# Performance work log

Hardware: AMD Instinct MI355X
Metric: run time of the kernel (lower is better)

The kernel has to match this reference:

```python
import jax, jax.numpy as jnp
import numpy as np

ITERATIONS = 10      # skil_loss default
BORDER_SIZE = 25     # skil_loss default -> 51-tap gaussian
SIGMA = 10.0         # skil_loss default
LOSS_WEIGHT = 1.0
EPS = 1e-6


def _max_pool3(x):
    # 3x3 max pool, stride 1, SAME padding over last two dims of (N, H, W)
    return jax.lax.reduce_window(x, -jnp.inf, jax.lax.max,
                                 (1, 3, 3), (1, 1, 1), 'SAME')


def _soft_erode(x):
    return -_max_pool3(-x)


def _soft_dilate(x):
    return _max_pool3(x)


def _soft_open(x):
    return _soft_dilate(_soft_erode(x))


def soft_skeletonize(img, iterations):
    # clDice-style iterative soft skeletonization
    skel = jax.nn.relu(img - _soft_open(img))

    def body(carry, _):
        img, skel = carry
        img = _soft_erode(img)
        delta = jax.nn.relu(img - _soft_open(img))
        skel = skel + jax.nn.relu(delta - skel * delta)
        return (img, skel), None

    (img, skel), _ = jax.lax.scan(body, (img, skel), None, length=iterations)
    return skel


def apply_smooth_gaussian_diffusion(x, border_size, sigma):
    # Separable gaussian conv, kernel size 2*border_size+1, peak value 1
    # (soft dilation of the skeleton into a border band), clipped to [0, 1].
    r = jnp.arange(-border_size, border_size + 1, dtype=x.dtype)
    g = jnp.exp(-(r * r) / (2.0 * sigma * sigma))  # peak = 1 at center
    x4 = x[:, None, :, :]  # (N, 1, H, W)
    kh = g.reshape(1, 1, -1, 1)
    kw = g.reshape(1, 1, 1, -1)
    dn = ('NCHW', 'OIHW', 'NCHW')
    y = jax.lax.conv_general_dilated(x4, kh, (1, 1), 'SAME', dimension_numbers=dn)
    y = jax.lax.conv_general_dilated(y, kw, (1, 1), 'SAME', dimension_numbers=dn)
    return jnp.clip(y[:, 0], 0.0, 1.0)


def soft_dice(gt, pr, epsilon=EPS):
    num = 2.0 * jnp.sum(gt * pr, axis=(-2, -1))
    den = jnp.sum(gt * gt, axis=(-2, -1)) + jnp.sum(pr * pr, axis=(-2, -1))
    return (num + epsilon) / (den + epsilon)


def skil_loss(pred_fg, target):
    gt_skel = soft_skeletonize(target, ITERATIONS)
    pr_skel = soft_skeletonize(pred_fg, ITERATIONS)
    gt_border = apply_smooth_gaussian_diffusion(gt_skel, BORDER_SIZE, SIGMA)
    pr_border = apply_smooth_gaussian_diffusion(pr_skel, BORDER_SIZE, SIGMA)
    return 1.0 - soft_dice(gt_border, pr_border)  # (N,)


def setup_inputs() -> dict:
    key = jax.random.key(0)
    k1, k2 = jax.random.split(key)
    pred = jax.random.normal(k1, (8, 2, 1024, 1024), dtype=jnp.float32)
    target = jax.random.uniform(k2, (8, 1024, 1024), dtype=jnp.float32)
    return {"pred": pred, "target": target}


def reference(pred, target):
    # SkilLoss.forward: softmax over classes, foreground channel to skil_loss,
    # weighted_loss 'mean' reduction over batch.
    probs = jax.nn.softmax(pred, axis=1)
    fg = probs[:, 1]  # (N, H, W)
    loss = skil_loss(fg, target)
    return LOSS_WEIGHT * jnp.mean(loss)
```

## Files before the change

kernel.cpp:

```cpp
#include <hip/hip_runtime.h>

#define H 1024
#define W 1024
#define HW (H*W)
#define NB 8
#define NIMG 16
#define BORDER 25
#define KLEN 51

__device__ __constant__ float GW[KLEN] = {
  0.04393693f, 0.05613476f, 0.07100535f, 0.08892162f, 0.11025053f,
  0.13533528f, 0.16447446f, 0.19789869f, 0.23574608f, 0.27803730f,
  0.32465247f, 0.37531110f, 0.42955736f, 0.48675226f, 0.54607442f,
  0.60653066f, 0.66697681f, 0.72614904f, 0.78270454f, 0.83527021f,
  0.88249690f, 0.92311635f, 0.95599748f, 0.98019867f, 0.99501248f,
  1.00000000f,
  0.99501248f, 0.98019867f, 0.95599748f, 0.92311635f, 0.88249690f,
  0.83527021f, 0.78270454f, 0.72614904f, 0.66697681f, 0.60653066f,
  0.54607442f, 0.48675226f, 0.42955736f, 0.37531110f, 0.32465247f,
  0.27803730f, 0.23574608f, 0.19789869f, 0.16447446f, 0.13533528f,
  0.11025053f, 0.08892162f, 0.07100535f, 0.05613476f, 0.04393693f
};

__device__ inline float m3n(float a,float b,float c){
  float d; asm("v_min3_f32 %0, %1, %2, %3" : "=v"(d) : "v"(a), "v"(b), "v"(c));
  return d;
}
__device__ inline float m3x(float a,float b,float c){
  float d; asm("v_max3_f32 %0, %1, %2, %3" : "=v"(d) : "v"(a), "v"(b), "v"(c));
  return d;
}

__device__ inline float dpp_shr1(float x){
  return __int_as_float(__builtin_amdgcn_mov_dpp(__float_as_int(x), 0x138, 0xf, 0xf, true));
}
__device__ inline float dpp_shl1(float x){
  return __int_as_float(__builtin_amdgcn_mov_dpp(__float_as_int(x), 0x130, 0xf, 0xf, true));
}

__device__ inline float4 hmin4(float4 C){
  float Lw = dpp_shr1(C.w);
  float Rx = dpp_shl1(C.x);
  float4 h;
  h.x=m3n(Lw ,C.x,C.y); h.y=m3n(C.x,C.y,C.z);
  h.z=m3n(C.y,C.z,C.w); h.w=m3n(C.z,C.w,Rx );
  return h;
}
__device__ inline float4 hmax4(float4 C){
  float Lw = dpp_shr1(C.w);
  float Rx = dpp_shl1(C.x);
  float4 h;
  h.x=m3x(Lw ,C.x,C.y); h.y=m3x(C.x,C.y,C.z);
  h.z=m3x(C.y,C.z,C.w); h.w=m3x(C.z,C.w,Rx );
  return h;
}
__device__ inline float4 vmin3(float4 a,float4 b,float4 c){
  float4 o; o.x=m3n(a.x,b.x,c.x); o.y=m3n(a.y,b.y,c.y);
            o.z=m3n(a.z,b.z,c.z); o.w=m3n(a.w,b.w,c.w); return o;
}
__device__ inline float4 vmax3(float4 a,float4 b,float4 c){
  float4 o; o.x=m3x(a.x,b.x,c.x); o.y=m3x(a.y,b.y,c.y);
            o.z=m3x(a.z,b.z,c.z); o.w=m3x(a.w,b.w,c.w); return o;
}
__device__ inline float4 msk4(float4 e, bool v){
  constexpr float NINF = -__builtin_huge_valf();
  float4 o; o.x=v?e.x:NINF; o.y=v?e.y:NINF; o.z=v?e.z:NINF; o.w=v?e.w:NINF;
  return o;
}

__global__ __launch_bounds__(512, 4)
void skel11_kernel(const float* __restrict__ pred, const float* __restrict__ targ,
                   float* __restrict__ S, double* __restrict__ sums,
                   unsigned* __restrict__ cnt)
{
  constexpr float PINF = __builtin_huge_valf();
  __shared__ float4 Xch[2][32][32];

  const int img = blockIdx.z;
  const int bx = blockIdx.x, by = blockIdx.y;

  if (bx==0 && by==0 && img==0) {
    if (threadIdx.x < 3*NB) sums[threadIdx.x] = 0.0;
    if (threadIdx.x == 3*NB) cnt[0] = 0u;
  }

  const int gx0 = bx*104 - 12, gy0 = by*72 - 12;
  const int tid = threadIdx.x;
  const int g = tid >> 5;
  const int j = tid & 31;
  const int wid = tid >> 6;
  const int R0 = 6*g;
  const int gxb = gx0 + 4*j;
  const bool xok = ((unsigned)gxb < (unsigned)W);
  const bool cenj = (j >= 3) && (j < 29);
  const bool allok = (gx0 >= 0) && (gx0 + 128 <= W) && (gy0 >= 0) && (gy0 + 96 <= H);
  const bool cwave = (wid >= 1) && (wid <= 6);

  const int ixm = (g>0)  ? 2*g-1 : 0;
  const int ixp = (g<15) ? 2*g+2 : 31;

  float4 I[6], s[6];
  bool yok[6];

  #pragma unroll
  for (int k=0;k<6;++k) {
    int gy = gy0 + R0 + k;
    yok[k] = ((unsigned)gy < (unsigned)H);
    float4 v = make_float4(PINF,PINF,PINF,PINF);
    if (yok[k] && xok) {
      size_t off = (size_t)gy*(W/4) + (gxb>>2);
      if (img < NB) {
        v = ((const float4*)targ)[(size_t)img*(HW/4)+off];
      } else {
        int b2 = img - NB;
        float4 p0 = ((const float4*)pred)[(size_t)(2*b2  )*(HW/4)+off];
        float4 p1 = ((const float4*)pred)[(size_t)(2*b2+1)*(HW/4)+off];
        v.x = 1.0f/(1.0f + __expf(p0.x - p1.x));
        v.y = 1.0f/(1.0f + __expf(p0.y - p1.y));
        v.z = 1.0f/(1.0f + __expf(p0.z - p1.z));
        v.w = 1.0f/(1.0f + __expf(p0.w - p1.w));
      }
    }
    I[k] = v;
  }

  #pragma unroll
  for (int u=0; u<11; ++u) {
    float4 h[6];
    #pragma unroll
    for (int k=0;k<6;++k) h[k] = hmin4(I[k]);
    Xch[0][2*g  ][j] = h[0];
    Xch[0][2*g+1][j] = h[5];
    float4 e[6];
    e[1]=vmin3(h[0],h[1],h[2]);
    e[2]=vmin3(h[1],h[2],h[3]);
    e[3]=vmin3(h[2],h[3],h[4]);
    e[4]=vmin3(h[3],h[4],h[5]);
    __syncthreads();
    float4 hm = Xch[0][ixm][j];
    float4 hp = Xch[0][ixp][j];
    e[0]=vmin3(hm  ,h[0],h[1]);
    e[5]=vmin3(h[4],h[5],hp  );

    float4 x[6];
    if (cwave) {
      if (allok) {
        #pragma unroll
        for (int k=0;k<6;++k) x[k] = hmax4(e[k]);
      } else {
        #pragma unroll
        for (int k=0;k<6;++k) x[k] = hmax4(msk4(e[k], xok && yok[k]));
      }
      Xch[1][2*g  ][j] = x[0];
      Xch[1][2*g+1][j] = x[5];
      #pragma unroll
      for (int k=1;k<5;++k) {
        float4 dl = vmax3(x[k-1], x[k], x[k+1]);
        float dx = fmaxf(I[k].x-dl.x,0.f), dy = fmaxf(I[k].y-dl.y,0.f);
        float dz = fmaxf(I[k].z-dl.z,0.f), dw = fmaxf(I[k].w-dl.w,0.f);
        if (u == 0) {
          s[k] = make_float4(dx,dy,dz,dw);
        } else {
          s[k].x += fmaxf(fmaf(-s[k].x, dx, dx), 0.f);
          s[k].y += fmaxf(fmaf(-s[k].y, dy, dy), 0.f);
          s[k].z += fmaxf(fmaf(-s[k].z, dz, dz), 0.f);
          s[k].w += fmaxf(fmaf(-s[k].w, dw, dw), 0.f);
        }
      }
    } else if (wid == 0) {
      float4 x5 = allok ? hmax4(e[5]) : hmax4(msk4(e[5], xok && yok[5]));
      Xch[1][2*g+1][j] = x5;
    } else {
      float4 x0 = allok ? hmax4(e[0]) : hmax4(msk4(e[0], xok && yok[0]));
      Xch[1][2*g  ][j] = x0;
    }
    __syncthreads();

    if (cwave) {
      float4 xm = Xch[1][2*g-1][j];
      float4 xp = Xch[1][2*g+2][j];
      #pragma unroll
      for (int k=0;k<6;k+=5) {
        float4 dl = (k==0) ? vmax3(xm, x[0], x[1]) : vmax3(x[4], x[5], xp);
        float dx = fmaxf(I[k].x-dl.x,0.f), dy = fmaxf(I[k].y-dl.y,0.f);
        float dz = fmaxf(I[k].z-dl.z,0.f), dw = fmaxf(I[k].w-dl.w,0.f);
        if (u == 0) {
          s[k] = make_float4(dx,dy,dz,dw);
        } else {
          s[k].x += fmaxf(fmaf(-s[k].x, dx, dx), 0.f);
          s[k].y += fmaxf(fmaf(-s[k].y, dy, dy), 0.f);
          s[k].z += fmaxf(fmaf(-s[k].z, dz, dz), 0.f);
          s[k].w += fmaxf(fmaf(-s[k].w, dw, dw), 0.f);
        }
      }
    }
    #pragma unroll
    for (int k=0;k<6;++k) I[k] = e[k];
  }

  if (cwave && cenj && gxb < W) {
    #pragma unroll
    for (int k=0;k<6;++k) {
      int gy = gy0 + R0 + k;
      if (gy < H)
        ((float4*)S)[(size_t)img*(HW/4) + (size_t)gy*(W/4) + (gxb>>2)] = s[k];
    }
  }
}

__global__ __launch_bounds__(256)
void blur_h_kernel(const float* __restrict__ Sin, float* __restrict__ D)
{
  const int img = blockIdx.y;
  const int y = blockIdx.x;
  const int q = threadIdx.x;
  const float4* src = (const float4*)(Sin + (size_t)img*HW + (size_t)y*W);
  float a0=0.f, a1=0.f, a2=0.f, a3=0.f;
#define ACCUM(val, idx)                                                     \
  { if ((idx)   >= 0 && (idx)   <= 50) a0 += (val) * GW[(idx)];             \
    if ((idx)-1 >= 0 && (idx)-1 <= 50) a1 += (val) * GW[(idx)-1];           \
    if ((idx)-2 >= 0 && (idx)-2 <= 50) a2 += (val) * GW[(idx)-2];           \
    if ((idx)-3 >= 0 && (idx)-3 <= 50) a3 += (val) * GW[(idx)-3]; }
  #pragma unroll
  for (int c = -7; c <= 7; ++c) {
    int qq = q + c;
    float4 v = make_float4(0.f,0.f,0.f,0.f);
    if ((unsigned)qq < 256u) v = src[qq];
    const int base = 4*c + 25;
    ACCUM(v.x, base+0) ACCUM(v.y, base+1) ACCUM(v.z, base+2) ACCUM(v.w, base+3)
  }
#undef ACCUM
  float4 outv; outv.x=a0; outv.y=a1; outv.z=a2; outv.w=a3;
  ((float4*)(D + (size_t)img*HW + (size_t)y*W))[q] = outv;
}

#define NVB (16*16*NB)
__global__ __launch_bounds__(256)
void blur_v_dice_kernel(const float* __restrict__ D, double* __restrict__ sums,
                        unsigned* __restrict__ cnt, float* __restrict__ out)
{
  __shared__ double rbuf[12];
  const int b = blockIdx.z;
  const int gy0 = blockIdx.y * 64;
  const int gx0 = blockIdx.x * 64;
  const int tid = threadIdx.x;
  const int c  = tid & 63;
  const int r0 = gy0 + (tid >> 6) * 16;
  const int x  = gx0 + c;
  const float* gsrc = D + (size_t)b*HW + x;
  const float* psrc = D + (size_t)(b+NB)*HW + x;

  float ag[16], ap[16];
  #pragma unroll
  for (int j = 0; j < 16; ++j) { ag[j] = 0.f; ap[j] = 0.f; }
  #pragma unroll
  for (int t = 0; t < 16 + KLEN - 1; ++t) {
    int gy = r0 - BORDER + t;
    float vg = 0.f, vp = 0.f;
    if ((unsigned)gy < (unsigned)H) {
      size_t a = (size_t)gy*W;
      vg = gsrc[a]; vp = psrc[a];
    }
    #pragma unroll
    for (int j = 0; j < 16; ++j) {
      int k = t - j;
      if (k >= 0 && k < KLEN) { ag[j] += vg * GW[k]; ap[j] += vp * GW[k]; }
    }
  }
  double sgp = 0.0, sgg = 0.0, spp = 0.0;
  #pragma unroll
  for (int j = 0; j < 16; ++j) {
    float a = fminf(fmaxf(ag[j], 0.f), 1.f);
    float p = fminf(fmaxf(ap[j], 0.f), 1.f);
    sgp += (double)(a*p); sgg += (double)(a*a); spp += (double)(p*p);
  }
  #pragma unroll
  for (int off = 32; off > 0; off >>= 1) {
    sgp += __shfl_down(sgp, off);
    sgg += __shfl_down(sgg, off);
    spp += __shfl_down(spp, off);
  }
  int lane = tid & 63, wv = tid >> 6;
  if (lane == 0) { rbuf[wv] = sgp; rbuf[4+wv] = sgg; rbuf[8+wv] = spp; }
  __syncthreads();
  if (tid == 0) {
    double a  = rbuf[0]+rbuf[1]+rbuf[2]+rbuf[3];
    double g2 = rbuf[4]+rbuf[5]+rbuf[6]+rbuf[7];
    double p2 = rbuf[8]+rbuf[9]+rbuf[10]+rbuf[11];
    atomicAdd(&sums[b],        a);
    atomicAdd(&sums[NB+b],     g2);
    atomicAdd(&sums[2*NB+b],   p2);
    __threadfence();
    unsigned done = atomicAdd(cnt, 1u);
    if (done == NVB - 1) {
      __threadfence();
      double acc = 0.0;
      for (int bb = 0; bb < NB; ++bb) {
        double num = 2.0*sums[bb] + 1e-6;
        double den = sums[NB+bb] + sums[2*NB+bb] + 1e-6;
        acc += 1.0 - num/den;
      }
      out[0] = (float)(acc / (double)NB);
    }
  }
}

extern "C" void kernel_launch(void* const* d_in, const int* in_sizes, int n_in,
                              void* d_out, int out_size, void* d_ws, size_t ws_size,
                              hipStream_t stream)
{
  (void)in_sizes; (void)n_in; (void)out_size; (void)ws_size;
  const float* pred = (const float*)d_in[0];
  const float* targ = (const float*)d_in[1];
  float* out = (float*)d_out;

  float* Ybuf = (float*)d_ws;
  float* Sbuf = Ybuf + (size_t)NIMG*HW;
  double* sums = (double*)(Sbuf + (size_t)NIMG*HW);
  unsigned* cnt = (unsigned*)(sums + 3*NB);

  hipLaunchKernelGGL(skel11_kernel, dim3(10, 15, NIMG), dim3(512), 0, stream,
                     pred, targ, Sbuf, sums, cnt);
  hipLaunchKernelGGL(blur_h_kernel, dim3(H, NIMG), dim3(256), 0, stream, Sbuf, Ybuf);
  hipLaunchKernelGGL(blur_v_dice_kernel, dim3(W/64, H/64, NB), dim3(256), 0, stream,
                     Ybuf, sums, cnt, out);
}
```

Baseline: 244.0 us.

## Fuse horizontal and vertical blur with dice via shared-memory ring buffer

Merges the horizontal blur kernel and the vertical blur plus dice kernel into one kernel. Each block computes horizontally blurred rows into a 128-row shared-memory ring buffer for both gt and pred, then runs the vertical 51-tap blur and dice partial sums from shared memory. This removes the full-size intermediate write and read of 16 blurred images in global memory. In exchange the grid shrinks to 512 blocks with serialized row strips, which lowers parallelism and adds a block-wide sync per strip.

Measured after the change: 205.4 us. -15.8%, faster.

```diff
diff --git a/kernel.cpp b/kernel.cpp
--- a/kernel.cpp
+++ b/kernel.cpp
@@ -208,72 +208,94 @@
   }
 }
 
-__global__ __launch_bounds__(256)
-void blur_h_kernel(const float* __restrict__ Sin, float* __restrict__ D)
+#define NVB (16*4*NB)
+__global__ __launch_bounds__(256, 2)
+void blurdice_kernel(const float* __restrict__ Sin, double* __restrict__ sums,
+                     unsigned* __restrict__ cnt, float* __restrict__ out)
 {
-  const int img = blockIdx.y;
-  const int y = blockIdx.x;
-  const int q = threadIdx.x;
-  const float4* src = (const float4*)(Sin + (size_t)img*HW + (size_t)y*W);
-  float a0=0.f, a1=0.f, a2=0.f, a3=0.f;
-#define ACCUM(val, idx)                                                     \
+  __shared__ float HbG[128][64];
+  __shared__ float HbP[128][64];
+  __shared__ double rbuf[12];
+
+  const int sx = blockIdx.x;
+  const int vh = blockIdx.y;
+  const int b  = blockIdx.z;
+  const int tid = threadIdx.x;
+  const int R0 = vh * 256;
+
+  const float* G0 = Sin + (size_t)b*HW;
+  const float* P0 = Sin + (size_t)(b+NB)*HW;
+
+  const int pr = tid >> 4;
+  const int pc = tid & 15;
+  const int qg = sx*16 + pc;
+
+  const int vg = tid >> 6;
+  const int vc = tid & 63;
+
+  double sgp = 0.0, sgg = 0.0, spp = 0.0;
+
+#define HACC(val, idx)                                                      \
   { if ((idx)   >= 0 && (idx)   <= 50) a0 += (val) * GW[(idx)];             \
     if ((idx)-1 >= 0 && (idx)-1 <= 50) a1 += (val) * GW[(idx)-1];           \
     if ((idx)-2 >= 0 && (idx)-2 <= 50) a2 += (val) * GW[(idx)-2];           \
     if ((idx)-3 >= 0 && (idx)-3 <= 50) a3 += (val) * GW[(idx)-3]; }
+
+#define HROW(SRC, DST, ROW)                                                 \
+  { float a0=0.f, a1=0.f, a2=0.f, a3=0.f;                                   \
+    if ((unsigned)(ROW) < (unsigned)H) {                                    \
+      const float4* s4 = (const float4*)((SRC) + (size_t)(ROW)*W);          \
+      _Pragma("unroll")                                                     \
+      for (int coff = -7; coff <= 7; ++coff) {                              \
+        int qq = qg + coff;                                                 \
+        float4 v = make_float4(0.f,0.f,0.f,0.f);                            \
+        if ((unsigned)qq < 256u) v = s4[qq];                                \
+        const int base = 4*coff + 25;                                       \
+        HACC(v.x, base+0) HACC(v.y, base+1) HACC(v.z, base+2) HACC(v.w, base+3) \
+      }                                                                     \
+    }                                                                       \
+    float4 hv; hv.x=a0; hv.y=a1; hv.z=a2; hv.w=a3;                          \
+    *(float4*)&DST[((ROW)+128)&127][4*pc] = hv; }
+
   #pragma unroll
-  for (int c = -7; c <= 7; ++c) {
-    int qq = q + c;
-    float4 v = make_float4(0.f,0.f,0.f,0.f);
-    if ((unsigned)qq < 256u) v = src[qq];
-    const int base = 4*c + 25;
-    ACCUM(v.x, base+0) ACCUM(v.y, base+1) ACCUM(v.z, base+2) ACCUM(v.w, base+3)
-  }
-#undef ACCUM
-  float4 outv; outv.x=a0; outv.y=a1; outv.z=a2; outv.w=a3;
-  ((float4*)(D + (size_t)img*HW + (size_t)y*W))[q] = outv;
-}
-
-#define NVB (16*16*NB)
-__global__ __launch_bounds__(256)
-void blur_v_dice_kernel(const float* __restrict__ D, double* __restrict__ sums,
-                        unsigned* __restrict__ cnt, float* __restrict__ out)
-{
-  __shared__ double rbuf[12];
-  const int b = blockIdx.z;
-  const int gy0 = blockIdx.y * 64;
-  const int gx0 = blockIdx.x * 64;
-  const int tid = threadIdx.x;
-  const int c  = tid & 63;
-  const int r0 = gy0 + (tid >> 6) * 16;
-  const int x  = gx0 + c;
-  const float* gsrc = D + (size_t)b*HW + x;
-  const float* psrc = D + (size_t)(b+NB)*HW + x;
-
-  float ag[16], ap[16];
-  #pragma unroll
-  for (int j = 0; j < 16; ++j) { ag[j] = 0.f; ap[j] = 0.f; }
-  #pragma unroll
-  for (int t = 0; t < 16 + KLEN - 1; ++t) {
-    int gy = r0 - BORDER + t;
-    float vg = 0.f, vp = 0.f;
-    if ((unsigned)gy < (unsigned)H) {
-      size_t a = (size_t)gy*W;
-      vg = gsrc[a]; vp = psrc[a];
-    }
-    #pragma unroll
-    for (int j = 0; j < 16; ++j) {
-      int k = t - j;
-      if (k >= 0 && k < KLEN) { ag[j] += vg * GW[k]; ap[j] += vp * GW[k]; }
-    }
-  }
-  double sgp = 0.0, sgg = 0.0, spp = 0.0;
-  #pragma unroll
-  for (int j = 0; j < 16; ++j) {
-    float a = fminf(fmaxf(ag[j], 0.f), 1.f);
-    float p = fminf(fmaxf(ap[j], 0.f), 1.f);
-    sgp += (double)(a*p); sgg += (double)(a*a); spp += (double)(p*p);
-  }
+  for (int p = 0; p < 4; ++p) {
+    int row = R0 - 39 + 16*p + pr;
+    HROW(G0, HbG, row)
+    HROW(P0, HbP, row)
+  }
+  __syncthreads();
+
+  for (int t = 0; t < 16; ++t) {
+    const int R = R0 + 16*t;
+    {
+      int row = R + 25 + pr;
+      HROW(G0, HbG, row)
+      HROW(P0, HbP, row)
+    }
+    __syncthreads();
+    float ag[4] = {0.f,0.f,0.f,0.f}, ap[4] = {0.f,0.f,0.f,0.f};
+    #pragma unroll
+    for (int tt = 0; tt < 54; ++tt) {
+      int ry  = R + 4*vg - 25 + tt;
+      int idx = (ry + 128) & 127;
+      float hg = HbG[idx][vc];
+      float hp = HbP[idx][vc];
+      #pragma unroll
+      for (int jj = 0; jj < 4; ++jj) {
+        int k = tt - jj;
+        if (k >= 0 && k < KLEN) { ag[jj] += hg * GW[k]; ap[jj] += hp * GW[k]; }
+      }
+    }
+    #pragma unroll
+    for (int jj = 0; jj < 4; ++jj) {
+      float a = fminf(fmaxf(ag[jj], 0.f), 1.f);
+      float p = fminf(fmaxf(ap[jj], 0.f), 1.f);
+      sgp += (double)(a*p); sgg += (double)(a*a); spp += (double)(p*p);
+    }
+  }
+#undef HROW
+#undef HACC
+
   #pragma unroll
   for (int off = 32; off > 0; off >>= 1) {
     sgp += __shfl_down(sgp, off);
@@ -287,9 +309,9 @@
     double a  = rbuf[0]+rbuf[1]+rbuf[2]+rbuf[3];
     double g2 = rbuf[4]+rbuf[5]+rbuf[6]+rbuf[7];
     double p2 = rbuf[8]+rbuf[9]+rbuf[10]+rbuf[11];
-    atomicAdd(&sums[b],        a);
-    atomicAdd(&sums[NB+b],     g2);
-    atomicAdd(&sums[2*NB+b],   p2);
+    atomicAdd(&sums[b],      a);
+    atomicAdd(&sums[NB+b],   g2);
+    atomicAdd(&sums[2*NB+b], p2);
     __threadfence();
     unsigned done = atomicAdd(cnt, 1u);
     if (done == NVB - 1) {
@@ -314,14 +336,12 @@
   const float* targ = (const float*)d_in[1];
   float* out = (float*)d_out;
 
-  float* Ybuf = (float*)d_ws;
-  float* Sbuf = Ybuf + (size_t)NIMG*HW;
+  float* Sbuf = (float*)d_ws;
   double* sums = (double*)(Sbuf + (size_t)NIMG*HW);
   unsigned* cnt = (unsigned*)(sums + 3*NB);
 
   hipLaunchKernelGGL(skel11_kernel, dim3(10, 15, NIMG), dim3(512), 0, stream,
                      pred, targ, Sbuf, sums, cnt);
-  hipLaunchKernelGGL(blur_h_kernel, dim3(H, NIMG), dim3(256), 0, stream, Sbuf, Ybuf);
-  hipLaunchKernelGGL(blur_v_dice_kernel, dim3(W/64, H/64, NB), dim3(256), 0, stream,
-                     Ybuf, sums, cnt, out);
-}
+  hipLaunchKernelGGL(blurdice_kernel, dim3(16, 4, NB), dim3(256), 0, stream,
+                     Sbuf, sums, cnt, out);
+}
```
